# Optimization experiments

Measured on AMD Instinct MI355X. Metric: run time of the kernel, lower is better.

Reference implementation:

```python
import jax, jax.numpy as jnp
import numpy as np

DECAY = 0.1
ALPHA = 0.2
EPS = 1e-8


def setup_inputs() -> dict:
    key = jax.random.key(0)
    k1, k2, k3, k4 = jax.random.split(key, 4)
    B, S, N, V = 8, 1024, 64, 32000
    input_ids = jax.random.randint(k1, (B, S), 0, V)
    emb = jax.random.normal(k2, (V, N), dtype=jnp.float32)
    W = jax.random.normal(k3, (N, N, N), dtype=jnp.float32) * 0.05
    Wd = jax.random.normal(k4, (V, N), dtype=jnp.float32) * 0.02
    bd = jnp.zeros((V,), dtype=jnp.float32)
    return {"input_ids": input_ids, "emb": emb, "W": W, "Wd": Wd, "bd": bd}


def reference(input_ids, emb, W, Wd, bd):
    B, S = input_ids.shape
    N = W.shape[0]
    # Precompute relu(embedding) for all timesteps: [B, S, N]
    word = jax.nn.relu(emb[input_ids])

    def step(hidden, w_t):
        # hidden, w_t: [B, N]
        x = (1.0 - DECAY) * hidden + w_t
        interaction = jnp.einsum('ijk,bi,bj->bk', W, x, x)
        x_act = jax.nn.relu(x + ALPHA * interaction)
        h = x_act / (jnp.sum(x_act, axis=1, keepdims=True) + EPS)
        return h, h

    h0 = jnp.zeros((B, N), dtype=emb.dtype)
    hT, hs = jax.lax.scan(step, h0, jnp.swapaxes(word, 0, 1))  # hs: [S, B, N]
    # Decode every step: Linear(N -> V): h @ Wd.T + bd -> [B, S, V]
    logits = jnp.einsum('sbn,vn->bsv', hs, Wd) + bd
    return logits, hT
```

## Files before the change

kernel.cpp:

```cpp
#include <hip/hip_runtime.h>


typedef unsigned int u32;
typedef unsigned short u16;
typedef __attribute__((ext_vector_type(8))) short short8;
typedef __attribute__((ext_vector_type(4))) float f32x4;
typedef __attribute__((ext_vector_type(4))) int i32x4;

#define DECAY_ 0.1f
#define ALPHA_ 0.2f
#define EPS_ 1e-8f
#define B_ 8
#define S_ 1024
#define N_ 64
#define V_ 32000
#define NCHUNK_ 32
#define CHUNK_ 32
#define WARM_ 12
#define UBOUND_ 0.45f
#define NUNITS_ 288
#define UQ_DWORDS_ (NUNITS_ * 64 * 2)

static __device__ __forceinline__ u16 f2bf(float f) {
  u32 u = __float_as_uint(f);
  u32 r = (u + 0x7fffu + ((u >> 16) & 1u)) >> 16;
  return (u16)r;
}

#if defined(__has_builtin)
#if __has_builtin(__builtin_amdgcn_sdot4)
#define HAVE_SDOT4 1
#endif
#endif
static __device__ __forceinline__ int dot4(int a, int b, int c) {
#ifdef HAVE_SDOT4
  return __builtin_amdgcn_sdot4(a, b, c, false);
#else
  int s = c;
  s += (int)(signed char)(a) * (int)(signed char)(b);
  s += (int)(signed char)(a >> 8) * (int)(signed char)(b >> 8);
  s += (int)(signed char)(a >> 16) * (int)(signed char)(b >> 16);
  s += (int)(a >> 24) * (int)(b >> 24);
  return s;
#endif
}

static __device__ __forceinline__ float wave_max64(float v) {
#pragma unroll
  for (int m = 1; m < 64; m <<= 1) v = fmaxf(v, __shfl_xor(v, m, 64));
  return v;
}

__global__ void prep_kernel(const float* __restrict__ Wd, u16* __restrict__ wdb,
                            const float* __restrict__ W, u32* __restrict__ Uq) {
  int idx = blockIdx.x * blockDim.x + threadIdx.x;
  wdb[idx] = f2bf(Wd[idx]);
  if (blockIdx.x < 64) {
    const int j = blockIdx.x;
    const int m = j >> 3;
    const int off8 = j + 4 * m * (m - 1) + (j & 7) * m;
    const int cnt = 2 * (m + 1) * 64;
    const float s = 127.0f / UBOUND_;
    for (int d = threadIdx.x; d < cnt; d += 256) {
      int q4 = d >> 6;
      int k = d & 63;
      u32 pk = 0;
#pragma unroll
      for (int e = 0; e < 4; ++e) {
        int i = 4 * q4 + e;
        float v = 0.0f;
        if (i < j)
          v = W[((size_t)i * N_ + j) * N_ + k] + W[((size_t)j * N_ + i) * N_ + k];
        else if (i == j)
          v = W[((size_t)j * N_ + j) * N_ + k];
        int qi = (int)rintf(v * s);
        qi = qi > 127 ? 127 : (qi < -127 ? -127 : qi);
        pk |= ((u32)qi & 0xffu) << (8 * e);
      }
      int dst = 2 * ((off8 + (q4 >> 1)) * 64 + k) + (q4 & 1);
      Uq[dst] = pk;
    }
  }
}

__global__ __launch_bounds__(512, 2) void recur_kernel(
    const int* __restrict__ ids, const float* __restrict__ emb,
    const u32* __restrict__ Uq,
    u16* __restrict__ hs, float* __restrict__ outHT) {
  const int b = blockIdx.y;
  const int chunk = blockIdx.x;
  const int lane = threadIdx.x & 63;
  const int w = threadIdx.x >> 6;

  const int t0 = chunk * CHUNK_;
  const int ts = (chunk == 0) ? 0 : t0 - WARM_;
  const int tend = t0 + CHUNK_;

  __shared__ int2 lw2[NUNITS_ * 64];
  __shared__ float part[8 * 64];
  __shared__ float xf_lds[N_];
  __shared__ u32 xq_lds[16];
  __shared__ float pend_w[2][N_];
  __shared__ float pend_b[2];

  const float sW = UBOUND_ * (1.0f / 127.0f);

  {
    const i32x4* src = (const i32x4*)Uq;
    i32x4* dst = (i32x4*)lw2;
    for (int ii = threadIdx.x; ii < UQ_DWORDS_ / 4; ii += 512) dst[ii] = src[ii];
  }

  float xk = 0.0f, smul = 0.0f;

  if (w == 0) {
    int id0 = ids[b * S_ + ts];
    xk = fmaxf(emb[(size_t)id0 * N_ + lane], 0.0f);
    float bnd = fmaxf(wave_max64(xk), 1e-20f);
    smul = bnd * (1.0f / 127.0f) * sW;
    float inv = 127.0f / bnd;
    float u = xk * inv;
    float u0 = __shfl(u, (lane & 15) * 4 + 0, 64);
    float u1 = __shfl(u, (lane & 15) * 4 + 1, 64);
    float u2 = __shfl(u, (lane & 15) * 4 + 2, 64);
    float u3 = __shfl(u, (lane & 15) * 4 + 3, 64);
    xf_lds[lane] = xk;
    if (lane < 16) {
      xq_lds[lane] = (u32)(int)rintf(u0) | ((u32)(int)rintf(u1) << 8) |
                     ((u32)(int)rintf(u2) << 16) | ((u32)(int)rintf(u3) << 24);
    }
  }
  if (w == 1) {
    int i1 = ts + 1 < S_ ? ts + 1 : S_ - 1;
    int id1 = ids[b * S_ + i1];
    float pv = fmaxf(emb[(size_t)id1 * N_ + lane], 0.0f);
    float pm = wave_max64(pv);
    pend_w[(ts + 1) & 1][lane] = pv;
    if (lane == 0) pend_b[(ts + 1) & 1] = pm;
  }
  __syncthreads();

  for (int t = ts; t < tend; ++t) {
    float pv = 0.0f;
    if (w == 1) {
      int i2 = t + 2 < S_ ? t + 2 : S_ - 1;
      pv = emb[(size_t)ids[b * S_ + i2] * N_ + lane];
    }
    u32 pkv = xq_lds[lane & 15];
    int xr[16];
#pragma unroll
    for (int q = 0; q < 16; ++q) xr[q] = __builtin_amdgcn_readlane((int)pkv, q);
    float pf = 0.0f;
#pragma unroll
    for (int m = 0; m < 8; ++m) {
      const int j = w + 8 * m;
      const int off8 = j + 4 * m * (m - 1) + w * m;
      int a = 0;
#pragma unroll
      for (int u = 0; u <= m; ++u) {
        int2 v = lw2[(off8 + u) * 64 + lane];
        a = dot4(xr[2 * u], v.x, a);
        a = dot4(xr[2 * u + 1], v.y, a);
      }
      pf += (float)a * xf_lds[j];
    }
    part[(w << 6) | lane] = pf;
    __syncthreads();

    if (w == 0) {
      float iact = 0.0f;
#pragma unroll
      for (int q = 0; q < 8; ++q) iact += part[(q << 6) | lane];
      float xact = fmaxf(fmaf(ALPHA_ * smul, iact, xk), 0.0f);
      float s = xact;
#pragma unroll
      for (int m = 1; m < 64; m <<= 1) s += __shfl_xor(s, m, 64);
      float rS = 1.0f / (s + EPS_);
      float h = xact * rS;

      if (t >= t0) {
        hs[((size_t)b * S_ + t) * N_ + lane] = f2bf(h);
        if (t == S_ - 1) outHT[b * N_ + lane] = h;
      }

      int rs = (t + 1) & 1;
      float wn = pend_w[rs][lane];
      float xn = fmaf(1.0f - DECAY_, h, wn);
      float nbnd = (1.0f - DECAY_) + pend_b[rs];
      float inv = 127.0f / nbnd;
      float u = xn * inv;
      float u0 = __shfl(u, (lane & 15) * 4 + 0, 64);
      float u1 = __shfl(u, (lane & 15) * 4 + 1, 64);
      float u2 = __shfl(u, (lane & 15) * 4 + 2, 64);
      float u3 = __shfl(u, (lane & 15) * 4 + 3, 64);
      xf_lds[lane] = xn;
      if (lane < 16) {
        xq_lds[lane] = (u32)(int)rintf(u0) | ((u32)(int)rintf(u1) << 8) |
                       ((u32)(int)rintf(u2) << 16) | ((u32)(int)rintf(u3) << 24);
      }
      smul = nbnd * (1.0f / 127.0f) * sW;
      xk = xn;
    } else if (w == 1) {
      float pr = fmaxf(pv, 0.0f);
      float pm = wave_max64(pr);
      pend_w[t & 1][lane] = pr;
      if (lane == 0) pend_b[t & 1] = pm;
    }
    __syncthreads();
  }
}

__global__ __launch_bounds__(512, 2) void decode_kernel(
    const u16* __restrict__ hs, const u16* __restrict__ wd,
    const float* __restrict__ bd, float* __restrict__ out) {
  const int lane = threadIdx.x & 63;
  const int w = threadIdx.x >> 6;
  const int wm = w >> 2, wn = w & 3;
  const int n0 = blockIdx.x * 128 + wn * 32;
  const int m0 = blockIdx.y * 128 + wm * 64;
  const int kg = (lane >> 4) * 8;
  const int rl = lane & 15;

  short8 bfr[2][2];
#pragma unroll
  for (int nt = 0; nt < 2; ++nt) {
    int v = n0 + nt * 16 + rl;
#pragma unroll
    for (int ks = 0; ks < 2; ++ks)
      bfr[nt][ks] = *(const short8*)(wd + (size_t)v * N_ + ks * 32 + kg);
  }
  short8 a[4][2];
#pragma unroll
  for (int mt = 0; mt < 4; ++mt) {
    int row = m0 + mt * 16 + rl;
#pragma unroll
    for (int ks = 0; ks < 2; ++ks)
      a[mt][ks] = *(const short8*)(hs + (size_t)row * N_ + ks * 32 + kg);
  }
  f32x4 acc[4][2];
#pragma unroll
  for (int nt = 0; nt < 2; ++nt) {
    float bdv = bd[n0 + nt * 16 + rl];
#pragma unroll
    for (int mt = 0; mt < 4; ++mt) acc[mt][nt] = {bdv, bdv, bdv, bdv};
  }
#pragma unroll
  for (int mt = 0; mt < 4; ++mt)
#pragma unroll
    for (int nt = 0; nt < 2; ++nt) {
      acc[mt][nt] =
          __builtin_amdgcn_mfma_f32_16x16x32_bf16(a[mt][0], bfr[nt][0], acc[mt][nt], 0, 0, 0);
      acc[mt][nt] =
          __builtin_amdgcn_mfma_f32_16x16x32_bf16(a[mt][1], bfr[nt][1], acc[mt][nt], 0, 0, 0);
    }
#pragma unroll
  for (int mt = 0; mt < 4; ++mt) {
    int rbase = m0 + mt * 16 + (lane >> 4) * 4;
#pragma unroll
    for (int i = 0; i < 4; ++i) {
      float* op = out + (size_t)(rbase + i) * V_ + n0 + rl;
      __builtin_nontemporal_store(acc[mt][0][i], op);
      __builtin_nontemporal_store(acc[mt][1][i], op + 16);
    }
  }
}

extern "C" void kernel_launch(void* const* d_in, const int* in_sizes, int n_in,
                              void* d_out, int out_size, void* d_ws, size_t ws_size,
                              hipStream_t stream) {
  const int* ids = (const int*)d_in[0];
  const float* emb = (const float*)d_in[1];
  const float* W = (const float*)d_in[2];
  const float* Wd = (const float*)d_in[3];
  const float* bd = (const float*)d_in[4];
  float* out = (float*)d_out;
  char* ws = (char*)d_ws;

  u32* Uq = (u32*)(ws);
  u16* hs = (u16*)(ws + 147456);
  u16* wdb = (u16*)(ws + 1196032);

  hipLaunchKernelGGL(prep_kernel, dim3(8000), dim3(256), 0, stream, Wd, wdb, W, Uq);
  hipLaunchKernelGGL(recur_kernel, dim3(NCHUNK_, B_), dim3(512), 0, stream, ids, emb,
                     Uq, hs, out + (size_t)B_ * S_ * V_);
  hipLaunchKernelGGL(decode_kernel, dim3(V_ / 128, (B_ * S_) / 128), dim3(512), 0, stream,
                     hs, wdb, bd, out);

  (void)in_sizes; (void)n_in; (void)out_size; (void)ws_size;
}
```

Baseline: 296.7 us.

## Replicate recurrence epilogue across all waves to drop second barrier per step

Every wave now redundantly computes the reduction, normalization, next-state quantization and next embedding prefetch in registers, instead of wave 0 doing it and broadcasting through LDS. This removes the second __syncthreads per timestep and the LDS round-trips for xf/xq/pending embeddings. Double-buffering the partial-sum array keeps a single barrier safe. The cost is redundant VALU work, shuffles and extra global embedding loads in all eight waves.

```diff
diff --git a/kernel.cpp b/kernel.cpp
--- a/kernel.cpp
+++ b/kernel.cpp
@@ -97,11 +97,7 @@
   const int tend = t0 + CHUNK_;
 
   __shared__ int2 lw2[NUNITS_ * 64];
-  __shared__ float part[8 * 64];
-  __shared__ float xf_lds[N_];
-  __shared__ u32 xq_lds[16];
-  __shared__ float pend_w[2][N_];
-  __shared__ float pend_b[2];
+  __shared__ float part[2][8][64];
 
   const float sW = UBOUND_ * (1.0f / 127.0f);
 
@@ -111,9 +107,9 @@
     for (int ii = threadIdx.x; ii < UQ_DWORDS_ / 4; ii += 512) dst[ii] = src[ii];
   }
 
-  float xk = 0.0f, smul = 0.0f;
-
-  if (w == 0) {
+  float xk, smul;
+  u32 pk;
+  {
     int id0 = ids[b * S_ + ts];
     xk = fmaxf(emb[(size_t)id0 * N_ + lane], 0.0f);
     float bnd = fmaxf(wave_max64(xk), 1e-20f);
@@ -124,32 +120,24 @@
     float u1 = __shfl(u, (lane & 15) * 4 + 1, 64);
     float u2 = __shfl(u, (lane & 15) * 4 + 2, 64);
     float u3 = __shfl(u, (lane & 15) * 4 + 3, 64);
-    xf_lds[lane] = xk;
-    if (lane < 16) {
-      xq_lds[lane] = (u32)(int)rintf(u0) | ((u32)(int)rintf(u1) << 8) |
-                     ((u32)(int)rintf(u2) << 16) | ((u32)(int)rintf(u3) << 24);
-    }
-  }
-  if (w == 1) {
+    pk = (u32)(int)rintf(u0) | ((u32)(int)rintf(u1) << 8) |
+         ((u32)(int)rintf(u2) << 16) | ((u32)(int)rintf(u3) << 24);
+  }
+  float pcur, pmax;
+  {
     int i1 = ts + 1 < S_ ? ts + 1 : S_ - 1;
-    int id1 = ids[b * S_ + i1];
-    float pv = fmaxf(emb[(size_t)id1 * N_ + lane], 0.0f);
-    float pm = wave_max64(pv);
-    pend_w[(ts + 1) & 1][lane] = pv;
-    if (lane == 0) pend_b[(ts + 1) & 1] = pm;
+    pcur = fmaxf(emb[(size_t)ids[b * S_ + i1] * N_ + lane], 0.0f);
+    pmax = wave_max64(pcur);
   }
   __syncthreads();
 
   for (int t = ts; t < tend; ++t) {
-    float pv = 0.0f;
-    if (w == 1) {
-      int i2 = t + 2 < S_ ? t + 2 : S_ - 1;
-      pv = emb[(size_t)ids[b * S_ + i2] * N_ + lane];
-    }
-    u32 pkv = xq_lds[lane & 15];
+    int i2 = t + 2 < S_ ? t + 2 : S_ - 1;
+    float praw = emb[(size_t)ids[b * S_ + i2] * N_ + lane];
+
     int xr[16];
 #pragma unroll
-    for (int q = 0; q < 16; ++q) xr[q] = __builtin_amdgcn_readlane((int)pkv, q);
+    for (int q = 0; q < 16; ++q) xr[q] = __builtin_amdgcn_readlane((int)pk, q);
     float pf = 0.0f;
 #pragma unroll
     for (int m = 0; m < 8; ++m) {
@@ -162,51 +150,43 @@
         a = dot4(xr[2 * u], v.x, a);
         a = dot4(xr[2 * u + 1], v.y, a);
       }
-      pf += (float)a * xf_lds[j];
-    }
-    part[(w << 6) | lane] = pf;
+      float xj = __uint_as_float(
+          __builtin_amdgcn_readlane(__float_as_uint(xk), j));
+      pf += (float)a * xj;
+    }
+    part[t & 1][w][lane] = pf;
     __syncthreads();
 
-    if (w == 0) {
-      float iact = 0.0f;
-#pragma unroll
-      for (int q = 0; q < 8; ++q) iact += part[(q << 6) | lane];
-      float xact = fmaxf(fmaf(ALPHA_ * smul, iact, xk), 0.0f);
-      float s = xact;
-#pragma unroll
-      for (int m = 1; m < 64; m <<= 1) s += __shfl_xor(s, m, 64);
-      float rS = 1.0f / (s + EPS_);
-      float h = xact * rS;
-
-      if (t >= t0) {
-        hs[((size_t)b * S_ + t) * N_ + lane] = f2bf(h);
-        if (t == S_ - 1) outHT[b * N_ + lane] = h;
-      }
-
-      int rs = (t + 1) & 1;
-      float wn = pend_w[rs][lane];
-      float xn = fmaf(1.0f - DECAY_, h, wn);
-      float nbnd = (1.0f - DECAY_) + pend_b[rs];
-      float inv = 127.0f / nbnd;
-      float u = xn * inv;
-      float u0 = __shfl(u, (lane & 15) * 4 + 0, 64);
-      float u1 = __shfl(u, (lane & 15) * 4 + 1, 64);
-      float u2 = __shfl(u, (lane & 15) * 4 + 2, 64);
-      float u3 = __shfl(u, (lane & 15) * 4 + 3, 64);
-      xf_lds[lane] = xn;
-      if (lane < 16) {
-        xq_lds[lane] = (u32)(int)rintf(u0) | ((u32)(int)rintf(u1) << 8) |
-                       ((u32)(int)rintf(u2) << 16) | ((u32)(int)rintf(u3) << 24);
-      }
-      smul = nbnd * (1.0f / 127.0f) * sW;
-      xk = xn;
-    } else if (w == 1) {
-      float pr = fmaxf(pv, 0.0f);
-      float pm = wave_max64(pr);
-      pend_w[t & 1][lane] = pr;
-      if (lane == 0) pend_b[t & 1] = pm;
-    }
-    __syncthreads();
+    float iact = 0.0f;
+#pragma unroll
+    for (int q = 0; q < 8; ++q) iact += part[t & 1][q][lane];
+    float xact = fmaxf(fmaf(ALPHA_ * smul, iact, xk), 0.0f);
+    float s = xact;
+#pragma unroll
+    for (int m = 1; m < 64; m <<= 1) s += __shfl_xor(s, m, 64);
+    float rS = 1.0f / (s + EPS_);
+    float h = xact * rS;
+
+    if (w == 0 && t >= t0) {
+      hs[((size_t)b * S_ + t) * N_ + lane] = f2bf(h);
+      if (t == S_ - 1) outHT[b * N_ + lane] = h;
+    }
+
+    float xn = fmaf(1.0f - DECAY_, h, pcur);
+    float nbnd = (1.0f - DECAY_) + pmax;
+    float inv = 127.0f / nbnd;
+    float u = xn * inv;
+    float u0 = __shfl(u, (lane & 15) * 4 + 0, 64);
+    float u1 = __shfl(u, (lane & 15) * 4 + 1, 64);
+    float u2 = __shfl(u, (lane & 15) * 4 + 2, 64);
+    float u3 = __shfl(u, (lane & 15) * 4 + 3, 64);
+    pk = (u32)(int)rintf(u0) | ((u32)(int)rintf(u1) << 8) |
+         ((u32)(int)rintf(u2) << 16) | ((u32)(int)rintf(u3) << 24);
+    smul = nbnd * (1.0f / 127.0f) * sW;
+    xk = xn;
+
+    pcur = fmaxf(praw, 0.0f);
+    pmax = wave_max64(pcur);
   }
 }
 
```

Result: no change. 302.4 us (+1.9%).
